# Optimization experiments

Measured on AMD Instinct MI355X. Metric: run time of the kernel, lower is better.

Reference implementation:

```python
import jax, jax.numpy as jnp
import numpy as np

N_NODES = 100000
N_EDGES = 1600000
D = 128


def setup_inputs() -> dict:
    key = jax.random.key(0)
    ks = jax.random.split(key, 8)
    x = jax.random.normal(ks[0], (N_NODES, D), dtype=jnp.float32)
    edge_index = jax.random.randint(ks[1], (2, N_EDGES), 0, N_NODES, dtype=jnp.int64)
    # Linear weights ~ fan-in scaled init
    scale = 1.0 / np.sqrt(D)
    W1 = jax.random.normal(ks[2], (D, D), dtype=jnp.float32) * scale
    W2 = jax.random.normal(ks[3], (D, D), dtype=jnp.float32) * scale
    W3 = jax.random.normal(ks[4], (D, D), dtype=jnp.float32) * scale
    b1 = jnp.zeros((D,), jnp.float32)
    b2 = jnp.zeros((D,), jnp.float32)
    b3 = jnp.zeros((D,), jnp.float32)
    # train_eps=True, PyG initializes eps to 0
    eps1 = jnp.zeros((), jnp.float32)
    eps2 = jnp.zeros((), jnp.float32)
    eps3 = jnp.zeros((), jnp.float32)
    return {"x": x, "edge_index": edge_index,
            "W1": W1, "b1": b1, "eps1": eps1,
            "W2": W2, "b2": b2, "eps2": eps2,
            "W3": W3, "b3": b3, "eps3": eps3}


def _gin_conv(x, src, dst, eps, W, b):
    # scatter-add neighbor aggregation: sum_{j in N(i)} x_j
    agg = jax.ops.segment_sum(x[src], dst, num_segments=N_NODES)  # [N, D]
    h = (1.0 + eps) * x + agg
    return jax.nn.relu(h @ W + b)


def reference(x, edge_index, W1, b1, eps1, W2, b2, eps2, W3, b3, eps3):
    src, dst = edge_index[0], edge_index[1]
    h = _gin_conv(x, src, dst, eps1, W1, b1)   # conv1 (dropout p=0 -> identity)
    h = _gin_conv(h, src, dst, eps2, W2, b2)
    h = _gin_conv(h, src, dst, eps3, W3, b3)
    return jax.nn.log_softmax(h, axis=1)
```

## Files before the change

kernel.cpp:

```cpp
#include <hip/hip_runtime.h>
#include <hip/hip_bf16.h>

#define N_NODES 100000
#define N_EDGES 1600000
#define D 128
#define NRANGE 8
#define RANGE_SZ 12500
#define SB_PER_RANGE 196
#define NBUCKET (NRANGE * SB_PER_RANGE)
#define G_PART 512
#define CH_PART 3125

typedef __attribute__((ext_vector_type(8))) short bf16x8;
typedef __attribute__((ext_vector_type(8))) unsigned short u16x8;
typedef __attribute__((ext_vector_type(4))) float f32x4;
typedef unsigned int u32;

__device__ inline ushort f2b(float x) {
    union { float f; unsigned u; } v; v.f = x;
    unsigned r = (v.u + 0x7fff + ((v.u >> 16) & 1)) >> 16;
    return (ushort)r;
}
__device__ inline float b2f(ushort b) {
    union { unsigned u; float f; } v; v.u = ((unsigned)b) << 16;
    return v.f;
}

__global__ void x2b_kernel(const float* __restrict__ x, ushort* __restrict__ xb) {
    int i = blockIdx.x * blockDim.x + threadIdx.x;
    if (i >= N_NODES * D / 4) return;
    float4 v = ((const float4*)x)[i];
    ushort4 o;
    o.x = f2b(v.x); o.y = f2b(v.y); o.z = f2b(v.z); o.w = f2b(v.w);
    ((ushort4*)xb)[i] = o;
}


__global__ void hist1_kernel(const int* __restrict__ dst, int* __restrict__ bhist1) {
    __shared__ int lh[NRANGE];
    if (threadIdx.x < NRANGE) lh[threadIdx.x] = 0;
    __syncthreads();
    int s0 = blockIdx.x * CH_PART, s1 = s0 + CH_PART;
    if (s1 > N_EDGES) s1 = N_EDGES;
    for (int i = s0 + threadIdx.x; i < s1; i += 256)
        atomicAdd(&lh[dst[i] / RANGE_SZ], 1);
    __syncthreads();
    if (threadIdx.x < NRANGE) bhist1[blockIdx.x * NRANGE + threadIdx.x] = lh[threadIdx.x];
}

__global__ void scan1_kernel(const int* __restrict__ bhist1, int* __restrict__ cbase1,
                             int* __restrict__ rs) {
    int r = threadIdx.x >> 6, lane = threadIdx.x & 63;
    __shared__ int rtot[NRANGE], roff[NRANGE];
    int excl[8];
    int run = 0;
    #pragma unroll
    for (int seg = 0; seg < 8; ++seg) {
        int b = seg * 64 + lane;
        int v = bhist1[b * NRANGE + r];
        int sc = v;
        #pragma unroll
        for (int off = 1; off < 64; off <<= 1) {
            int y = __shfl_up(sc, off);
            if (lane >= off) sc += y;
        }
        excl[seg] = run + sc - v;
        run += __shfl(sc, 63);
    }
    if (lane == 63) rtot[r] = run;
    __syncthreads();
    if (threadIdx.x == 0) {
        int a = 0;
        for (int i = 0; i < NRANGE; ++i) { roff[i] = a; a += rtot[i]; }
    }
    __syncthreads();
    int base = roff[r];
    #pragma unroll
    for (int seg = 0; seg < 8; ++seg)
        cbase1[(seg * 64 + lane) * NRANGE + r] = base + excl[seg];
    if (threadIdx.x < NRANGE) rs[threadIdx.x] = roff[threadIdx.x];
    if (threadIdx.x == 0) rs[NRANGE] = N_EDGES;
}

__global__ void place1_kernel(const int* __restrict__ src, const int* __restrict__ dst,
                              const int* __restrict__ cbase1, u32* __restrict__ epack1) {
    __shared__ int cur[NRANGE];
    if (threadIdx.x < NRANGE) cur[threadIdx.x] = cbase1[blockIdx.x * NRANGE + threadIdx.x];
    __syncthreads();
    int s0 = blockIdx.x * CH_PART, s1 = s0 + CH_PART;
    if (s1 > N_EDGES) s1 = N_EDGES;
    for (int i = s0 + threadIdx.x; i < s1; i += 256) {
        int d = dst[i], s = src[i];
        int r = d / RANGE_SZ;
        int dl = d - r * RANGE_SZ;
        int p = atomicAdd(&cur[r], 1);
        epack1[p] = ((u32)dl << 17) | (u32)s;
    }
}

__global__ void hist2_kernel(const u32* __restrict__ epack1, const int* __restrict__ rs,
                             int* __restrict__ bhist2) {
    __shared__ int lh[SB_PER_RANGE];
    for (int i = threadIdx.x; i < SB_PER_RANGE; i += 256) lh[i] = 0;
    __syncthreads();
    int r = blockIdx.x >> 6, j = blockIdx.x & 63;
    int e0 = rs[r], e1 = rs[r + 1];
    int cs = (e1 - e0 + 63) >> 6;
    int s0 = e0 + j * cs, s1 = s0 + cs;
    if (s1 > e1) s1 = e1;
    for (int i = s0 + threadIdx.x; i < s1; i += 256)
        atomicAdd(&lh[epack1[i] >> 23], 1);
    __syncthreads();
    for (int i = threadIdx.x; i < SB_PER_RANGE; i += 256)
        bhist2[blockIdx.x * SB_PER_RANGE + i] = lh[i];
}

__global__ void scan2_kernel(const int* __restrict__ bhist2, const int* __restrict__ rs,
                             int* __restrict__ cbase2, int* __restrict__ bucket_start) {
    int r = blockIdx.x;
    __shared__ int tot[SB_PER_RANGE];
    __shared__ int base[SB_PER_RANGE];
    int sb = threadIdx.x;
    if (sb < SB_PER_RANGE) {
        int s = 0;
        for (int j = 0; j < 64; ++j) s += bhist2[(r * 64 + j) * SB_PER_RANGE + sb];
        tot[sb] = s;
    }
    __syncthreads();
    if (threadIdx.x == 0) {
        int a = 0;
        for (int i = 0; i < SB_PER_RANGE; ++i) { base[i] = a; a += tot[i]; }
    }
    __syncthreads();
    if (sb < SB_PER_RANGE) {
        int run = rs[r] + base[sb];
        bucket_start[r * SB_PER_RANGE + sb] = run;
        for (int j = 0; j < 64; ++j) {
            cbase2[(r * 64 + j) * SB_PER_RANGE + sb] = run;
            run += bhist2[(r * 64 + j) * SB_PER_RANGE + sb];
        }
    }
    if (r == NRANGE - 1 && threadIdx.x == 0) bucket_start[NBUCKET] = N_EDGES;
}

__global__ void place2_kernel(const u32* __restrict__ epack1, const int* __restrict__ rs,
                              const int* __restrict__ cbase2, u32* __restrict__ epack2) {
    __shared__ int cur[SB_PER_RANGE];
    for (int i = threadIdx.x; i < SB_PER_RANGE; i += 256)
        cur[i] = cbase2[blockIdx.x * SB_PER_RANGE + i];
    __syncthreads();
    int r = blockIdx.x >> 6, j = blockIdx.x & 63;
    int e0 = rs[r], e1 = rs[r + 1];
    int cs = (e1 - e0 + 63) >> 6;
    int s0 = e0 + j * cs, s1 = s0 + cs;
    if (s1 > e1) s1 = e1;
    for (int i = s0 + threadIdx.x; i < s1; i += 256) {
        u32 e = epack1[i];
        int sb = e >> 23;
        int p = atomicAdd(&cur[sb], 1);
        epack2[p] = e & 0x7FFFFFu;
    }
}

__global__ void sort3_kernel(const u32* __restrict__ epack2, const int* __restrict__ bucket_start,
                             int* __restrict__ row_ptr, int* __restrict__ col) {
    int b = blockIdx.x;
    int r = b / SB_PER_RANGE, sb = b - r * SB_PER_RANGE;
    int node_base = r * RANGE_SZ + sb * 64;
    int nb = r * RANGE_SZ + RANGE_SZ - node_base;
    if (nb > 64) nb = 64;
    int e0 = bucket_start[b], e1 = bucket_start[b + 1];
    __shared__ int hist[64], cur[64];
    if (threadIdx.x < 64) hist[threadIdx.x] = 0;
    __syncthreads();
    for (int i = e0 + threadIdx.x; i < e1; i += 256)
        atomicAdd(&hist[(epack2[i] >> 17) & 63], 1);
    __syncthreads();
    if (threadIdx.x < 64) {
        int v = hist[threadIdx.x];
        int sc = v;
        #pragma unroll
        for (int off = 1; off < 64; off <<= 1) {
            int y = __shfl_up(sc, off);
            if (threadIdx.x >= off) sc += y;
        }
        int ex = e0 + sc - v;
        cur[threadIdx.x] = ex;
        if (threadIdx.x < nb) row_ptr[node_base + threadIdx.x] = ex;
    }
    __syncthreads();
    for (int i = e0 + threadIdx.x; i < e1; i += 256) {
        u32 e = epack2[i];
        int l = (e >> 17) & 63;
        int p = atomicAdd(&cur[l], 1);
        col[p] = (int)(e & 0x1FFFFu);
    }
    if (b == NBUCKET - 1 && threadIdx.x == 0) row_ptr[N_NODES] = N_EDGES;
}


__global__ void aggregate_kernel(const ushort* __restrict__ xb, const int* __restrict__ row_ptr,
                                 const int* __restrict__ col, const float* __restrict__ eps_p,
                                 ushort* __restrict__ hb) {
    int gt = blockIdx.x * blockDim.x + threadIdx.x;
    int node = gt >> 4;
    if (node >= N_NODES) return;
    int l16 = threadIdx.x & 15;
    int beg = row_ptr[node], end = row_ptr[node + 1];
    float a0[8] = {0,0,0,0,0,0,0,0};
    float a1[8] = {0,0,0,0,0,0,0,0};
    int e = beg;
    for (; e + 7 < end; e += 8) {
        int s[8];
        #pragma unroll
        for (int j = 0; j < 8; ++j) s[j] = col[e + j];
        u16x8 v[8];
        #pragma unroll
        for (int j = 0; j < 8; ++j)
            v[j] = *(const u16x8*)(xb + ((size_t)s[j] << 7) + l16 * 8);
        #pragma unroll
        for (int j = 0; j < 8; ++j) {
            float* a = (j & 1) ? a1 : a0;
            #pragma unroll
            for (int k = 0; k < 8; ++k) a[k] += b2f(v[j][k]);
        }
    }
    for (; e < end; ++e) {
        int s = col[e];
        u16x8 v = *(const u16x8*)(xb + ((size_t)s << 7) + l16 * 8);
        #pragma unroll
        for (int k = 0; k < 8; ++k) a0[k] += b2f(v[k]);
    }
    float scale = 1.0f + *eps_p;
    u16x8 xi = *(const u16x8*)(xb + ((size_t)node << 7) + l16 * 8);
    u16x8 ho;
    #pragma unroll
    for (int k = 0; k < 8; ++k) {
        float o = a0[k] + a1[k] + scale * b2f(xi[k]);
        ho[k] = f2b(o);
    }
    *(u16x8*)(hb + ((size_t)node << 7) + l16 * 8) = ho;
}

__global__ void wsplit_kernel(const float* __restrict__ W, ushort* __restrict__ wt_hi,
                              ushort* __restrict__ wt_lo) {
    int t = blockIdx.x * blockDim.x + threadIdx.x;
    if (t >= D * D) return;
    int k = t >> 7, n = t & 127;
    float w = W[t];
    ushort hi = f2b(w);
    ushort lo = f2b(w - b2f(hi));
    wt_hi[n * D + k] = hi;
    wt_lo[n * D + k] = lo;
}

template <bool BF16OUT>
__launch_bounds__(256, 2)
__global__ void gemm_relu_mfma(const ushort* __restrict__ hb,
                               const ushort* __restrict__ wt_hi, const ushort* __restrict__ wt_lo,
                               const float* __restrict__ bias,
                               float* __restrict__ outf, ushort* __restrict__ outb) {
    int wv = threadIdx.x >> 6, lane = threadIdx.x & 63;
    int r0 = blockIdx.x * 128 + wv * 32;
    int arow = lane & 15, agrp = lane >> 4;
    bf16x8 Ah[2][4];
    #pragma unroll
    for (int mf = 0; mf < 2; ++mf) {
        size_t rbase = (size_t)(r0 + mf * 16 + arow) * D;
        #pragma unroll
        for (int kf = 0; kf < 4; ++kf)
            Ah[mf][kf] = *(const bf16x8*)(hb + rbase + kf * 32 + agrp * 8);
    }
    f32x4 acc[2][8];
    #pragma unroll
    for (int mf = 0; mf < 2; ++mf)
        #pragma unroll
        for (int nf = 0; nf < 8; ++nf)
            acc[mf][nf] = (f32x4){0.f, 0.f, 0.f, 0.f};
    #pragma unroll
    for (int nf = 0; nf < 8; ++nf) {
        #pragma unroll
        for (int kf = 0; kf < 4; ++kf) {
            size_t wb = (size_t)(nf * 16 + arow) * D + kf * 32 + agrp * 8;
            bf16x8 bh = *(const bf16x8*)(wt_hi + wb);
            bf16x8 bl = *(const bf16x8*)(wt_lo + wb);
            #pragma unroll
            for (int mf = 0; mf < 2; ++mf) {
                acc[mf][nf] = __builtin_amdgcn_mfma_f32_16x16x32_bf16(Ah[mf][kf], bh, acc[mf][nf], 0, 0, 0);
                acc[mf][nf] = __builtin_amdgcn_mfma_f32_16x16x32_bf16(Ah[mf][kf], bl, acc[mf][nf], 0, 0, 0);
            }
        }
    }
    int crow = agrp * 4;
    #pragma unroll
    for (int mf = 0; mf < 2; ++mf) {
        #pragma unroll
        for (int nf = 0; nf < 8; ++nf) {
            int coln = nf * 16 + arow;
            float b = bias[coln];
            #pragma unroll
            for (int r = 0; r < 4; ++r) {
                int row = r0 + mf * 16 + crow + r;
                if (row < N_NODES) {
                    float val = fmaxf(acc[mf][nf][r] + b, 0.f);
                    if (BF16OUT) outb[(size_t)row * D + coln] = f2b(val);
                    else         outf[(size_t)row * D + coln] = val;
                }
            }
        }
    }
}

__global__ void log_softmax_kernel(float* __restrict__ y) {
    int w = (blockIdx.x * blockDim.x + threadIdx.x) >> 6;
    if (w >= N_NODES) return;
    int lane = threadIdx.x & 63;
    float2* y2 = (float2*)y;
    float2 v = y2[(size_t)w * 64 + lane];
    float m = fmaxf(v.x, v.y);
    #pragma unroll
    for (int off = 32; off; off >>= 1) m = fmaxf(m, __shfl_xor(m, off));
    float s = expf(v.x - m) + expf(v.y - m);
    #pragma unroll
    for (int off = 32; off; off >>= 1) s += __shfl_xor(s, off);
    float lse = m + logf(s);
    v.x -= lse;
    v.y -= lse;
    y2[(size_t)w * 64 + lane] = v;
}

extern "C" void kernel_launch(void* const* d_in, const int* in_sizes, int n_in,
                              void* d_out, int out_size, void* d_ws, size_t ws_size,
                              hipStream_t stream) {
    (void)in_sizes; (void)n_in; (void)out_size; (void)ws_size;
    const float* x  = (const float*)d_in[0];
    const int*   ei = (const int*)d_in[1];
    const int*   src = ei;
    const int*   dst = ei + N_EDGES;
    const float* W1 = (const float*)d_in[2];
    const float* b1 = (const float*)d_in[3];
    const float* e1 = (const float*)d_in[4];
    const float* W2 = (const float*)d_in[5];
    const float* b2 = (const float*)d_in[6];
    const float* e2 = (const float*)d_in[7];
    const float* W3 = (const float*)d_in[8];
    const float* b3 = (const float*)d_in[9];
    const float* e3 = (const float*)d_in[10];
    float* out = (float*)d_out;

    char* ws = (char*)d_ws;
    int*    rs           = (int*)ws;
    int*    bucket_start = (int*)(ws + 1024);
    int*    bhist1       = (int*)(ws + 8192);
    int*    cbase1       = (int*)(ws + 24576);
    int*    bhist2       = (int*)(ws + 40960);
    int*    cbase2       = (int*)(ws + 458752);
    int*    row_ptr      = (int*)(ws + 880640);
    int*    col          = (int*)(ws + 1572864);
    ushort* wt_hi        = (ushort*)(ws + 8388608);
    ushort* wt_lo        = (ushort*)(ws + 8454144);
    ushort* xb           = (ushort*)(ws + 9437184);
    ushort* hb           = (ushort*)(ws + 35651584);
    u32*    epack1       = (u32*)(ws + 35651584);
    u32*    epack2       = (u32*)(ws + 42991616);

    x2b_kernel<<<(N_NODES * D / 4 + 255) / 256, 256, 0, stream>>>(x, xb);

    hist1_kernel<<<G_PART, 256, 0, stream>>>(dst, bhist1);
    scan1_kernel<<<1, 512, 0, stream>>>(bhist1, cbase1, rs);
    place1_kernel<<<G_PART, 256, 0, stream>>>(src, dst, cbase1, epack1);
    hist2_kernel<<<G_PART, 256, 0, stream>>>(epack1, rs, bhist2);
    scan2_kernel<<<NRANGE, 256, 0, stream>>>(bhist2, rs, cbase2, bucket_start);
    place2_kernel<<<G_PART, 256, 0, stream>>>(epack1, rs, cbase2, epack2);
    sort3_kernel<<<NBUCKET, 256, 0, stream>>>(epack2, bucket_start, row_ptr, col);

    const int aggGrid = (N_NODES * 16 + 255) / 256;
    const int gemmGrid = (N_NODES + 127) / 128;

    aggregate_kernel<<<aggGrid, 256, 0, stream>>>(xb, row_ptr, col, e1, hb);
    wsplit_kernel<<<64, 256, 0, stream>>>(W1, wt_hi, wt_lo);
    gemm_relu_mfma<true><<<gemmGrid, 256, 0, stream>>>(hb, wt_hi, wt_lo, b1, nullptr, xb);
    aggregate_kernel<<<aggGrid, 256, 0, stream>>>(xb, row_ptr, col, e2, hb);
    wsplit_kernel<<<64, 256, 0, stream>>>(W2, wt_hi, wt_lo);
    gemm_relu_mfma<true><<<gemmGrid, 256, 0, stream>>>(hb, wt_hi, wt_lo, b2, nullptr, xb);
    aggregate_kernel<<<aggGrid, 256, 0, stream>>>(xb, row_ptr, col, e3, hb);
    wsplit_kernel<<<64, 256, 0, stream>>>(W3, wt_hi, wt_lo);
    gemm_relu_mfma<false><<<gemmGrid, 256, 0, stream>>>(hb, wt_hi, wt_lo, b3, out, nullptr);

    log_softmax_kernel<<<(N_NODES * 64 + 255) / 256, 256, 0, stream>>>(out);
}
```

Baseline: 409.1 us.

## Degree-sort nodes for aggregation, fuse log_softmax into GEMM, batch weight split

Adds a counting sort of nodes by in-degree (histogram, scan, placement) so that aggregation wavefronts process nodes with similar edge counts, which reduces lane divergence. Adds a 4-edge unrolled tail step in the gather loop. Fuses log_softmax into the final GEMM epilogue using 16-lane shuffles, which removes a separate pass over the fp32 output. Merges the three weight-split launches into one. The cost is extra preprocessing kernels, plus an indirect perm lookup that scatters the hb writes.

Result: slower. 644.4 us (+57.5%).

```diff
diff --git a/kernel.cpp b/kernel.cpp
--- a/kernel.cpp
+++ b/kernel.cpp
@@ -163,7 +163,8 @@
 }
 
 __global__ void sort3_kernel(const u32* __restrict__ epack2, const int* __restrict__ bucket_start,
-                             int* __restrict__ row_ptr, int* __restrict__ col) {
+                             int* __restrict__ row_ptr, int* __restrict__ col,
+                             int* __restrict__ deg) {
     int b = blockIdx.x;
     int r = b / SB_PER_RANGE, sb = b - r * SB_PER_RANGE;
     int node_base = r * RANGE_SZ + sb * 64;
@@ -186,7 +187,10 @@
         }
         int ex = e0 + sc - v;
         cur[threadIdx.x] = ex;
-        if (threadIdx.x < nb) row_ptr[node_base + threadIdx.x] = ex;
+        if (threadIdx.x < nb) {
+            row_ptr[node_base + threadIdx.x] = ex;
+            deg[node_base + threadIdx.x] = v;
+        }
     }
     __syncthreads();
     for (int i = e0 + threadIdx.x; i < e1; i += 256) {
@@ -199,12 +203,45 @@
 }
 
 
+__global__ void deghist_kernel(const int* __restrict__ deg, int* __restrict__ gdh) {
+    __shared__ int lh[128];
+    if (threadIdx.x < 128) lh[threadIdx.x] = 0;
+    __syncthreads();
+    int i = blockIdx.x * blockDim.x + threadIdx.x;
+    if (i < N_NODES) atomicAdd(&lh[min(deg[i], 127)], 1);
+    __syncthreads();
+    if (threadIdx.x < 128 && lh[threadIdx.x]) atomicAdd(&gdh[threadIdx.x], lh[threadIdx.x]);
+}
+
+__global__ void degscan_kernel(const int* __restrict__ gdh, int* __restrict__ dcur) {
+    __shared__ int sh[128];
+    int t = threadIdx.x;
+    sh[t] = gdh[t];
+    __syncthreads();
+    if (t == 0) {
+        int run = 0;
+        for (int b = 127; b >= 0; --b) { int c = sh[b]; sh[b] = run; run += c; }
+    }
+    __syncthreads();
+    dcur[t] = sh[t];
+}
+
+__global__ void degplace_kernel(const int* __restrict__ deg, int* __restrict__ dcur,
+                                int* __restrict__ perm) {
+    int i = blockIdx.x * blockDim.x + threadIdx.x;
+    if (i < N_NODES) {
+        int p = atomicAdd(&dcur[min(deg[i], 127)], 1);
+        perm[p] = i;
+    }
+}
+
+
 __global__ void aggregate_kernel(const ushort* __restrict__ xb, const int* __restrict__ row_ptr,
-                                 const int* __restrict__ col, const float* __restrict__ eps_p,
-                                 ushort* __restrict__ hb) {
-    int gt = blockIdx.x * blockDim.x + threadIdx.x;
-    int node = gt >> 4;
-    if (node >= N_NODES) return;
+                                 const int* __restrict__ col, const int* __restrict__ perm,
+                                 const float* __restrict__ eps_p, ushort* __restrict__ hb) {
+    int q = (blockIdx.x * blockDim.x + threadIdx.x) >> 4;
+    if (q >= N_NODES) return;
+    int node = perm[q];
     int l16 = threadIdx.x & 15;
     int beg = row_ptr[node], end = row_ptr[node + 1];
     float a0[8] = {0,0,0,0,0,0,0,0};
@@ -225,6 +262,22 @@
             for (int k = 0; k < 8; ++k) a[k] += b2f(v[j][k]);
         }
     }
+    if (e + 3 < end) {
+        int s[4];
+        #pragma unroll
+        for (int j = 0; j < 4; ++j) s[j] = col[e + j];
+        u16x8 v[4];
+        #pragma unroll
+        for (int j = 0; j < 4; ++j)
+            v[j] = *(const u16x8*)(xb + ((size_t)s[j] << 7) + l16 * 8);
+        #pragma unroll
+        for (int j = 0; j < 4; ++j) {
+            float* a = (j & 1) ? a1 : a0;
+            #pragma unroll
+            for (int k = 0; k < 8; ++k) a[k] += b2f(v[j][k]);
+        }
+        e += 4;
+    }
     for (; e < end; ++e) {
         int s = col[e];
         u16x8 v = *(const u16x8*)(xb + ((size_t)s << 7) + l16 * 8);
@@ -242,19 +295,21 @@
     *(u16x8*)(hb + ((size_t)node << 7) + l16 * 8) = ho;
 }
 
-__global__ void wsplit_kernel(const float* __restrict__ W, ushort* __restrict__ wt_hi,
-                              ushort* __restrict__ wt_lo) {
-    int t = blockIdx.x * blockDim.x + threadIdx.x;
-    if (t >= D * D) return;
+__global__ void wsplit3_kernel(const float* __restrict__ W1, const float* __restrict__ W2,
+                               const float* __restrict__ W3,
+                               ushort* __restrict__ wt_hi, ushort* __restrict__ wt_lo) {
+    int layer = blockIdx.x >> 6;
+    int t = (blockIdx.x & 63) * 256 + threadIdx.x;
+    const float* W = layer == 0 ? W1 : layer == 1 ? W2 : W3;
     int k = t >> 7, n = t & 127;
     float w = W[t];
     ushort hi = f2b(w);
     ushort lo = f2b(w - b2f(hi));
-    wt_hi[n * D + k] = hi;
-    wt_lo[n * D + k] = lo;
-}
-
-template <bool BF16OUT>
+    wt_hi[layer * D * D + n * D + k] = hi;
+    wt_lo[layer * D * D + n * D + k] = lo;
+}
+
+template <int MODE>
 __launch_bounds__(256, 2)
 __global__ void gemm_relu_mfma(const ushort* __restrict__ hb,
                                const ushort* __restrict__ wt_hi, const ushort* __restrict__ wt_lo,
@@ -291,42 +346,53 @@
             }
         }
     }
-    int crow = agrp * 4;
-    #pragma unroll
-    for (int mf = 0; mf < 2; ++mf) {
-        #pragma unroll
-        for (int nf = 0; nf < 8; ++nf) {
-            int coln = nf * 16 + arow;
-            float b = bias[coln];
+    float bcol[8];
+    #pragma unroll
+    for (int nf = 0; nf < 8; ++nf) bcol[nf] = bias[nf * 16 + arow];
+    if (MODE == 0) {
+        int crow = agrp * 4;
+        #pragma unroll
+        for (int mf = 0; mf < 2; ++mf) {
             #pragma unroll
-            for (int r = 0; r < 4; ++r) {
-                int row = r0 + mf * 16 + crow + r;
-                if (row < N_NODES) {
-                    float val = fmaxf(acc[mf][nf][r] + b, 0.f);
-                    if (BF16OUT) outb[(size_t)row * D + coln] = f2b(val);
-                    else         outf[(size_t)row * D + coln] = val;
+            for (int nf = 0; nf < 8; ++nf) {
+                int coln = nf * 16 + arow;
+                #pragma unroll
+                for (int r = 0; r < 4; ++r) {
+                    int row = r0 + mf * 16 + crow + r;
+                    if (row < N_NODES)
+                        outb[(size_t)row * D + coln] = f2b(fmaxf(acc[mf][nf][r] + bcol[nf], 0.f));
                 }
             }
         }
-    }
-}
-
-__global__ void log_softmax_kernel(float* __restrict__ y) {
-    int w = (blockIdx.x * blockDim.x + threadIdx.x) >> 6;
-    if (w >= N_NODES) return;
-    int lane = threadIdx.x & 63;
-    float2* y2 = (float2*)y;
-    float2 v = y2[(size_t)w * 64 + lane];
-    float m = fmaxf(v.x, v.y);
-    #pragma unroll
-    for (int off = 32; off; off >>= 1) m = fmaxf(m, __shfl_xor(m, off));
-    float s = expf(v.x - m) + expf(v.y - m);
-    #pragma unroll
-    for (int off = 32; off; off >>= 1) s += __shfl_xor(s, off);
-    float lse = m + logf(s);
-    v.x -= lse;
-    v.y -= lse;
-    y2[(size_t)w * 64 + lane] = v;
+    } else {
+        #pragma unroll
+        for (int mf = 0; mf < 2; ++mf) {
+            #pragma unroll
+            for (int rr = 0; rr < 4; ++rr) {
+                float v[8];
+                #pragma unroll
+                for (int nf = 0; nf < 8; ++nf)
+                    v[nf] = fmaxf(acc[mf][nf][rr] + bcol[nf], 0.f);
+                float m = v[0];
+                #pragma unroll
+                for (int nf = 1; nf < 8; ++nf) m = fmaxf(m, v[nf]);
+                #pragma unroll
+                for (int off = 1; off < 16; off <<= 1) m = fmaxf(m, __shfl_xor(m, off));
+                float s = 0.f;
+                #pragma unroll
+                for (int nf = 0; nf < 8; ++nf) s += __expf(v[nf] - m);
+                #pragma unroll
+                for (int off = 1; off < 16; off <<= 1) s += __shfl_xor(s, off);
+                float lse = m + __logf(s);
+                int row = r0 + mf * 16 + agrp * 4 + rr;
+                if (row < N_NODES) {
+                    #pragma unroll
+                    for (int nf = 0; nf < 8; ++nf)
+                        outf[(size_t)row * D + nf * 16 + arow] = v[nf] - lse;
+                }
+            }
+        }
+    }
 }
 
 extern "C" void kernel_launch(void* const* d_in, const int* in_sizes, int n_in,
@@ -354,11 +420,15 @@
     int*    bhist1       = (int*)(ws + 8192);
     int*    cbase1       = (int*)(ws + 24576);
     int*    bhist2       = (int*)(ws + 40960);
-    int*    cbase2       = (int*)(ws + 458752);
-    int*    row_ptr      = (int*)(ws + 880640);
-    int*    col          = (int*)(ws + 1572864);
-    ushort* wt_hi        = (ushort*)(ws + 8388608);
-    ushort* wt_lo        = (ushort*)(ws + 8454144);
+    int*    cbase2       = (int*)(ws + 442368);
+    int*    row_ptr      = (int*)(ws + 851968);
+    int*    deg          = (int*)(ws + 1253376);
+    int*    perm         = (int*)(ws + 1654784);
+    int*    gdh          = (int*)(ws + 2055168);
+    int*    dcur         = (int*)(ws + 2056192);
+    int*    col          = (int*)(ws + 2097152);
+    ushort* wt_hi        = (ushort*)(ws + 8519680);
+    ushort* wt_lo        = (ushort*)(ws + 8617984);
     ushort* xb           = (ushort*)(ws + 9437184);
     ushort* hb           = (ushort*)(ws + 35651584);
     u32*    epack1       = (u32*)(ws + 35651584);
@@ -372,20 +442,22 @@
     hist2_kernel<<<G_PART, 256, 0, stream>>>(epack1, rs, bhist2);
     scan2_kernel<<<NRANGE, 256, 0, stream>>>(bhist2, rs, cbase2, bucket_start);
     place2_kernel<<<G_PART, 256, 0, stream>>>(epack1, rs, cbase2, epack2);
-    sort3_kernel<<<NBUCKET, 256, 0, stream>>>(epack2, bucket_start, row_ptr, col);
+    sort3_kernel<<<NBUCKET, 256, 0, stream>>>(epack2, bucket_start, row_ptr, col, deg);
+
+    hipMemsetAsync(gdh, 0, 128 * sizeof(int), stream);
+    deghist_kernel<<<(N_NODES + 255) / 256, 256, 0, stream>>>(deg, gdh);
+    degscan_kernel<<<1, 128, 0, stream>>>(gdh, dcur);
+    degplace_kernel<<<(N_NODES + 255) / 256, 256, 0, stream>>>(deg, dcur, perm);
+
+    wsplit3_kernel<<<192, 256, 0, stream>>>(W1, W2, W3, wt_hi, wt_lo);
 
     const int aggGrid = (N_NODES * 16 + 255) / 256;
     const int gemmGrid = (N_NODES + 127) / 128;
 
-    aggregate_kernel<<<aggGrid, 256, 0, stream>>>(xb, row_ptr, col, e1, hb);
-    wsplit_kernel<<<64, 256, 0, stream>>>(W1, wt_hi, wt_lo);
-    gemm_relu_mfma<true><<<gemmGrid, 256, 0, stream>>>(hb, wt_hi, wt_lo, b1, nullptr, xb);
-    aggregate_kernel<<<aggGrid, 256, 0, stream>>>(xb, row_ptr, col, e2, hb);
-    wsplit_kernel<<<64, 256, 0, stream>>>(W2, wt_hi, wt_lo);
-    gemm_relu_mfma<true><<<gemmGrid, 256, 0, stream>>>(hb, wt_hi, wt_lo, b2, nullptr, xb);
-    aggregate_kernel<<<aggGrid, 256, 0, stream>>>(xb, row_ptr, col, e3, hb);
-    wsplit_kernel<<<64, 256, 0, stream>>>(W3, wt_hi, wt_lo);
-    gemm_relu_mfma<false><<<gemmGrid, 256, 0, stream>>>(hb, wt_hi, wt_lo, b3, out, nullptr);
-
-    log_softmax_kernel<<<(N_NODES * 64 + 255) / 256, 256, 0, stream>>>(out);
-}
+    aggregate_kernel<<<aggGrid, 256, 0, stream>>>(xb, row_ptr, col, perm, e1, hb);
+    gemm_relu_mfma<0><<<gemmGrid, 256, 0, stream>>>(hb, wt_hi, wt_lo, b1, nullptr, xb);
+    aggregate_kernel<<<aggGrid, 256, 0, stream>>>(xb, row_ptr, col, perm, e2, hb);
+    gemm_relu_mfma<0><<<gemmGrid, 256, 0, stream>>>(hb, wt_hi + D * D, wt_lo + D * D, b2, nullptr, xb);
+    aggregate_kernel<<<aggGrid, 256, 0, stream>>>(xb, row_ptr, col, perm, e3, hb);
+    gemm_relu_mfma<1><<<gemmGrid, 256, 0, stream>>>(hb, wt_hi + 2 * D * D, wt_lo + 2 * D * D, b3, out, nullptr);
+}
```
